# Performance work log

Hardware: AMD Instinct MI355X
Metric: run time of the kernel (lower is better)

The kernel has to match this reference:

```python
import jax, jax.numpy as jnp
import numpy as np
import math

D_MSA = 384
N_HEAD = 12
D_HID = 32


def setup_inputs() -> dict:
    key = jax.random.key(0)
    k1, k2, k3, k4, k5 = jax.random.split(key, 5)
    b, n, l = 2, 256, 384
    msa = jax.random.normal(k1, (b, n, l, D_MSA), dtype=jnp.float32)
    # xavier_uniform for (out, in) = (n_head*d_hidden, d_msa)
    fan_out, fan_in = N_HEAD * D_HID, D_MSA
    bound = math.sqrt(6.0 / (fan_in + fan_out))
    Wq = jax.random.uniform(k2, (fan_out, fan_in), jnp.float32, -bound, bound)
    Wk = jax.random.uniform(k3, (fan_out, fan_in), jnp.float32, -bound, bound)
    bq = jnp.zeros((fan_out,), jnp.float32)
    bk = jnp.zeros((fan_out,), jnp.float32)
    return {"msa": msa, "Wq": Wq, "bq": bq, "Wk": Wk, "bk": bk}


def reference(msa, Wq, bq, Wk, bk):
    b, n, l, _ = msa.shape
    scale = 1.0 / math.sqrt(D_HID)
    tar_seq = msa[:, 0]  # (b, l, d_msa) -- query comes from first MSA row
    q = (tar_seq @ Wq.T + bq).reshape(b, l, N_HEAD, D_HID) * scale  # (b,l,h,d)
    k = (msa @ Wk.T + bk).reshape(b, n, l, N_HEAD, D_HID)           # (b,n,l,h,d)
    # einsum('bqihd,bkihd->bkihq') with q==1 -> (b,n,l,h,1)
    attn = jnp.einsum('blhd,bnlhd->bnlh', q, k)[..., None]
    # softmax over MSA-depth axis (dim=1); dropout is identity at eval
    return jax.nn.softmax(attn, axis=1)
```

## Files before the change

kernel.cpp:

```cpp
#include <hip/hip_runtime.h>
#include <hip/hip_bf16.h>

#define D_MSA 384
#define NHEAD 12
#define DHID  32
#define BB    2
#define NN    256
#define LL    384
#define NBL   (BB * LL)
#define WFROW (NHEAD * D_MSA)

#define WF_OFF 0
#define WF_SZ  ((size_t)NBL * WFROW)
#define Q_OFF  (WF_OFF + WF_SZ)
#define Q_SZ   ((size_t)NBL * D_MSA)
#define CB_OFF (Q_OFF + Q_SZ)
#define CB_SZ  ((size_t)NBL * NHEAD)
#define LOG_OFF (CB_OFF + CB_SZ)
#define LOG_SZ ((size_t)NBL * NHEAD * NN)
#define WS_FLOATS (LOG_OFF + LOG_SZ)
#define WS_BYTES  (WS_FLOATS * 4)

__global__ __launch_bounds__(256)
void seqw_a1(const float* __restrict__ msa, const float* __restrict__ Wq,
             const float* __restrict__ bq, const float* __restrict__ bk,
             float* __restrict__ q_ws, float* __restrict__ cb_ws)
{
  __shared__ float tar[3][D_MSA];
  __shared__ float qs[3][D_MSA];
  const int t    = threadIdx.x;
  const int lane = t & 63;
  const int wv   = t >> 6;
  const int rowi = lane >> 4;
  const int seg  = lane & 15;
  const int bl0  = blockIdx.x * 3;
  const int b    = bl0 / LL, l0 = bl0 % LL;
  const float scale = 0.17677669529663687f;

  const float* base = msa + ((size_t)b * NN * LL + l0) * D_MSA;
  for (int i = t; i < 3 * D_MSA / 4; i += 256)
    ((float4*)tar)[i] = ((const float4*)base)[i];
  __syncthreads();

#pragma unroll 1
  for (int cc = 0; cc < 24; ++cc) {
    const int c = wv * 96 + cc * 4 + rowi;
    const float* wr = Wq + (size_t)c * D_MSA + seg * 4;
    float a0 = 0.f, a1 = 0.f, a2 = 0.f;
#pragma unroll
    for (int j = 0; j < 6; ++j) {
      float4 w4 = *(const float4*)(wr + 64 * j);
      float4 t0 = *(const float4*)&tar[0][64 * j + seg * 4];
      float4 t1 = *(const float4*)&tar[1][64 * j + seg * 4];
      float4 t2 = *(const float4*)&tar[2][64 * j + seg * 4];
      a0 = fmaf(w4.x, t0.x, a0); a0 = fmaf(w4.y, t0.y, a0);
      a0 = fmaf(w4.z, t0.z, a0); a0 = fmaf(w4.w, t0.w, a0);
      a1 = fmaf(w4.x, t1.x, a1); a1 = fmaf(w4.y, t1.y, a1);
      a1 = fmaf(w4.z, t1.z, a1); a1 = fmaf(w4.w, t1.w, a1);
      a2 = fmaf(w4.x, t2.x, a2); a2 = fmaf(w4.y, t2.y, a2);
      a2 = fmaf(w4.z, t2.z, a2); a2 = fmaf(w4.w, t2.w, a2);
    }
#pragma unroll
    for (int m = 8; m; m >>= 1) {
      a0 += __shfl_xor(a0, m);
      a1 += __shfl_xor(a1, m);
      a2 += __shfl_xor(a2, m);
    }
    if (seg == 0) {
      const float bqc = bq[c];
      const float q0 = scale * (a0 + bqc);
      const float q1 = scale * (a1 + bqc);
      const float q2 = scale * (a2 + bqc);
      qs[0][c] = q0; q_ws[(size_t)(bl0 + 0) * D_MSA + c] = q0;
      qs[1][c] = q1; q_ws[(size_t)(bl0 + 1) * D_MSA + c] = q1;
      qs[2][c] = q2; q_ws[(size_t)(bl0 + 2) * D_MSA + c] = q2;
    }
  }
  __syncthreads();

  if (t < 3 * NHEAD) {
    const int r = t / NHEAD, h = t % NHEAD;
    float s = 0.f;
#pragma unroll
    for (int d = 0; d < DHID; ++d)
      s = fmaf(qs[r][h * DHID + d], bk[h * DHID + d], s);
    cb_ws[(size_t)(bl0 + r) * NHEAD + h] = s;
  }
}

__global__ __launch_bounds__(256)
void seqw_a2(const float* __restrict__ Wk, const float* __restrict__ q_ws,
             float* __restrict__ wf_ws)
{
  __shared__ float qt[16][DHID];
  const int t   = threadIdx.x;
  const int h   = blockIdx.x % NHEAD;
  const int bl0 = (blockIdx.x / NHEAD) * 16;

  if (t < 128) {
    const int r = t >> 3, j = (t & 7) * 4;
    *(float4*)&qt[r][j] =
        *(const float4*)(q_ws + (size_t)(bl0 + r) * D_MSA + h * DHID + j);
  }
  __syncthreads();

#pragma unroll 1
  for (int pass = 0; pass < 2; ++pass) {
    const int c = pass * 256 + t;
    if (c < D_MSA) {
      float acc[16];
#pragma unroll
      for (int r = 0; r < 16; ++r) acc[r] = 0.f;
      const float* wkb = Wk + (size_t)(h * DHID) * D_MSA + c;
#pragma unroll 2
      for (int d = 0; d < DHID; d += 4) {
        const float w0 = wkb[(size_t)(d + 0) * D_MSA];
        const float w1 = wkb[(size_t)(d + 1) * D_MSA];
        const float w2 = wkb[(size_t)(d + 2) * D_MSA];
        const float w3 = wkb[(size_t)(d + 3) * D_MSA];
#pragma unroll
        for (int r = 0; r < 16; ++r) {
          float4 q4 = *(const float4*)&qt[r][d];
          acc[r] = fmaf(q4.x, w0, acc[r]);
          acc[r] = fmaf(q4.y, w1, acc[r]);
          acc[r] = fmaf(q4.z, w2, acc[r]);
          acc[r] = fmaf(q4.w, w3, acc[r]);
        }
      }
#pragma unroll
      for (int r = 0; r < 16; ++r)
        wf_ws[(size_t)(bl0 + r) * WFROW + h * D_MSA + c] = acc[r];
    }
  }
}

struct SmemB {
  float wf[NHEAD][D_MSA];
  float cb[NHEAD];
  float attn[NHEAD][128];
};

__global__ __launch_bounds__(256)
void seqw_b(const float* __restrict__ msa, const float* __restrict__ wf_ws,
            const float* __restrict__ cb_ws, float* __restrict__ log_ws)
{
  __shared__ SmemB sm;
  const int t    = threadIdx.x;
  const int lane = t & 63;
  const int wv   = t >> 6;
  const int rowi = lane >> 3;
  const int seg  = lane & 7;
  const int bid  = blockIdx.x;
  const int bl   = bid >> 1;
  const int nblk = bid & 1;
  const int b    = bl / LL;
  const int l    = bl - b * LL;
  const int h0   = 3 * wv;

  {
    const float4* src = (const float4*)(wf_ws + (size_t)bl * WFROW);
    for (int i = t; i < WFROW / 4; i += 256) ((float4*)sm.wf)[i] = src[i];
    if (t < NHEAD) sm.cb[t] = cb_ws[(size_t)bl * NHEAD + t];
  }
  __syncthreads();

  const size_t rstride = (size_t)LL * D_MSA;
  const float* lanebase =
      msa + ((size_t)(b * NN + nblk * 128 + rowi) * LL + l) * D_MSA + seg * 4;

#define LDB(buf, ch, j)                                                         \
  {                                                                             \
    _Pragma("unroll")                                                           \
    for (int g = 0; g < 8; ++g)                                                 \
      buf[g] = *(const float4*)(lanebase +                                      \
                 (size_t)((ch) * 64 + g * 8) * rstride + 32 * (j));             \
  }
#define CPB(buf, j)                                                             \
  {                                                                             \
    float4 w0 = *(const float4*)&sm.wf[h0 + 0][32 * (j) + 4 * seg];             \
    float4 w1 = *(const float4*)&sm.wf[h0 + 1][32 * (j) + 4 * seg];             \
    float4 w2 = *(const float4*)&sm.wf[h0 + 2][32 * (j) + 4 * seg];             \
    _Pragma("unroll")                                                           \
    for (int g = 0; g < 8; ++g) {                                               \
      acc[g][0] = fmaf(buf[g].x, w0.x, acc[g][0]);                              \
      acc[g][0] = fmaf(buf[g].y, w0.y, acc[g][0]);                              \
      acc[g][0] = fmaf(buf[g].z, w0.z, acc[g][0]);                              \
      acc[g][0] = fmaf(buf[g].w, w0.w, acc[g][0]);                              \
      acc[g][1] = fmaf(buf[g].x, w1.x, acc[g][1]);                              \
      acc[g][1] = fmaf(buf[g].y, w1.y, acc[g][1]);                              \
      acc[g][1] = fmaf(buf[g].z, w1.z, acc[g][1]);                              \
      acc[g][1] = fmaf(buf[g].w, w1.w, acc[g][1]);                              \
      acc[g][2] = fmaf(buf[g].x, w2.x, acc[g][2]);                              \
      acc[g][2] = fmaf(buf[g].y, w2.y, acc[g][2]);                              \
      acc[g][2] = fmaf(buf[g].z, w2.z, acc[g][2]);                              \
      acc[g][2] = fmaf(buf[g].w, w2.w, acc[g][2]);                              \
    }                                                                           \
  }

  float4 bufA[8], bufB[8];
  LDB(bufA, 0, 0)
#pragma unroll 1
  for (int ch = 0; ch < 2; ++ch) {
    float acc[8][3];
#pragma unroll
    for (int g = 0; g < 8; ++g) {
      acc[g][0] = 0.f; acc[g][1] = 0.f; acc[g][2] = 0.f;
    }
#pragma unroll 1
    for (int jj = 0; jj < 6; ++jj) {
      const int j0 = 2 * jj, j1 = 2 * jj + 1;
      LDB(bufB, ch, j1)
      CPB(bufA, j0)
      if (jj < 5)      LDB(bufA, ch, j0 + 2)
      else if (ch < 1) LDB(bufA, 1, 0)
      CPB(bufB, j1)
    }
#pragma unroll
    for (int g = 0; g < 8; ++g) {
#pragma unroll
      for (int hh = 0; hh < 3; ++hh) {
        float s = acc[g][hh];
        s += __shfl_xor(s, 4);
        s += __shfl_xor(s, 2);
        s += __shfl_xor(s, 1);
        if (seg == 0)
          sm.attn[h0 + hh][ch * 64 + g * 8 + rowi] = s + sm.cb[h0 + hh];
      }
    }
  }
  __syncthreads();

  for (int i = t; i < NHEAD * 128 / 4; i += 256) {
    const int h = i >> 5, nn4 = i & 31;
    ((float4*)log_ws)[(size_t)bl * (NHEAD * NN / 4) + h * (NN / 4) + nblk * 32 + nn4] =
        ((const float4*)sm.attn)[i];
  }
}

__global__ __launch_bounds__(256)
void seqw_c(const float* __restrict__ log_ws, float* __restrict__ out)
{
  __shared__ float at[NHEAD][NN];
  __shared__ float smax[NHEAD], sinv[NHEAD];
  const int t    = threadIdx.x;
  const int lane = t & 63;
  const int wv   = t >> 6;
  const int bl   = blockIdx.x;
  const int b    = bl / LL;
  const int l    = bl - b * LL;

  for (int i = t; i < NHEAD * NN / 4; i += 256)
    ((float4*)at)[i] = ((const float4*)log_ws)[(size_t)bl * (NHEAD * NN / 4) + i];
  __syncthreads();

#pragma unroll
  for (int jh = 0; jh < 3; ++jh) {
    const int h = wv * 3 + jh;
    float v0 = at[h][lane];
    float v1 = at[h][lane + 64];
    float v2 = at[h][lane + 128];
    float v3 = at[h][lane + 192];
    float mx = fmaxf(fmaxf(v0, v1), fmaxf(v2, v3));
#pragma unroll
    for (int m = 32; m; m >>= 1) mx = fmaxf(mx, __shfl_xor(mx, m));
    float s = __expf(v0 - mx) + __expf(v1 - mx) + __expf(v2 - mx) + __expf(v3 - mx);
#pragma unroll
    for (int m = 32; m; m >>= 1) s += __shfl_xor(s, m);
    if (lane == 0) { smax[h] = mx; sinv[h] = 1.0f / s; }
  }
  __syncthreads();

  {
    float o[NHEAD];
#pragma unroll
    for (int h = 0; h < NHEAD; ++h)
      o[h] = __expf(at[h][t] - smax[h]) * sinv[h];
    float* ob = out + ((size_t)(b * NN + t) * LL + l) * NHEAD;
    ((float4*)ob)[0] = make_float4(o[0], o[1], o[2],  o[3]);
    ((float4*)ob)[1] = make_float4(o[4], o[5], o[6],  o[7]);
    ((float4*)ob)[2] = make_float4(o[8], o[9], o[10], o[11]);
  }
}

struct SmemF {
  float tar[D_MSA];
  float q[D_MSA];
  float wf[NHEAD][D_MSA];
  float cb[NHEAD];
  float smax[NHEAD];
  float sinv[NHEAD];
  float attn[NHEAD][NN];
};

__global__ __launch_bounds__(512, 2)
void seqw_fused_fb(const float* __restrict__ msa, const float* __restrict__ Wq,
                   const float* __restrict__ bq, const float* __restrict__ Wk,
                   const float* __restrict__ bk, float* __restrict__ out)
{
  __shared__ SmemF sm;
  const int t    = threadIdx.x;
  const int lane = t & 63;
  const int wv   = t >> 6;
  const int rowi = lane >> 4;
  const int seg  = lane & 15;
  const int bl   = blockIdx.x;
  const int b    = bl / LL;
  const int l    = bl - b * LL;
  const float scale = 0.17677669529663687f;

  const float* targ = msa + ((size_t)(b * NN) * LL + l) * D_MSA;
  if (t < 96) ((float4*)sm.tar)[t] = ((const float4*)targ)[t];
  __syncthreads();

  {
    float2 t2[3];
#pragma unroll
    for (int p = 0; p < 3; ++p) t2[p] = *(const float2*)&sm.tar[2 * lane + 128 * p];
#pragma unroll 1
    for (int j = 0; j < 48; ++j) {
      const int r = wv * 48 + j;
      const float* wr = Wq + (size_t)r * D_MSA;
      float s = 0.f;
#pragma unroll
      for (int p = 0; p < 3; ++p) {
        float2 w2 = *(const float2*)&wr[2 * lane + 128 * p];
        s = fmaf(t2[p].x, w2.x, s);
        s = fmaf(t2[p].y, w2.y, s);
      }
#pragma unroll
      for (int m = 32; m; m >>= 1) s += __shfl_xor(s, m);
      if (lane == 0) sm.q[r] = scale * (s + bq[r]);
    }
  }
  __syncthreads();

  if (t < D_MSA) {
    const int c = t;
    float a[NHEAD];
#pragma unroll
    for (int h = 0; h < NHEAD; ++h) a[h] = 0.f;
#pragma unroll 1
    for (int d = 0; d < DHID; ++d) {
#pragma unroll
      for (int h = 0; h < NHEAD; ++h)
        a[h] = fmaf(sm.q[h * DHID + d], Wk[(size_t)(h * DHID + d) * D_MSA + c], a[h]);
    }
#pragma unroll
    for (int h = 0; h < NHEAD; ++h) sm.wf[h][c] = a[h];
  }
  if (t < NHEAD) {
    float s = 0.f;
#pragma unroll
    for (int d = 0; d < DHID; ++d) s = fmaf(sm.q[t * DHID + d], bk[t * DHID + d], s);
    sm.cb[t] = s;
  }
  __syncthreads();

  const size_t rstride = (size_t)LL * D_MSA;
  const float* lanebase =
      msa + ((size_t)(b * NN + wv * 32 + rowi) * LL + l) * D_MSA + seg * 4;

#define LDF(buf, base, j)                                                       \
  {                                                                             \
    buf[0] = *(const float4*)((base) + 64 * (j));                               \
    buf[1] = *(const float4*)((base) + 4 * rstride + 64 * (j));                 \
  }
#define CPF(buf, j)                                                             \
  {                                                                             \
    _Pragma("unroll")                                                           \
    for (int h = 0; h < NHEAD; ++h) {                                           \
      float4 w4 = *(const float4*)&sm.wf[h][64 * (j) + 4 * seg];                \
      acc[0][h] = fmaf(buf[0].x, w4.x, acc[0][h]);                              \
      acc[0][h] = fmaf(buf[0].y, w4.y, acc[0][h]);                              \
      acc[0][h] = fmaf(buf[0].z, w4.z, acc[0][h]);                              \
      acc[0][h] = fmaf(buf[0].w, w4.w, acc[0][h]);                              \
      acc[1][h] = fmaf(buf[1].x, w4.x, acc[1][h]);                              \
      acc[1][h] = fmaf(buf[1].y, w4.y, acc[1][h]);                              \
      acc[1][h] = fmaf(buf[1].z, w4.z, acc[1][h]);                              \
      acc[1][h] = fmaf(buf[1].w, w4.w, acc[1][h]);                              \
    }                                                                           \
  }

  const float* pcur = lanebase;
  float4 bufA[2], bufB[2];
  LDF(bufA, pcur, 0)
#pragma unroll 1
  for (int ch = 0; ch < 4; ++ch) {
    float acc[2][NHEAD];
#pragma unroll
    for (int g = 0; g < 2; ++g)
#pragma unroll
      for (int h = 0; h < NHEAD; ++h) acc[g][h] = 0.f;
    const float* pnext = pcur + 8 * rstride;
    LDF(bufB, pcur, 1)  CPF(bufA, 0)
    LDF(bufA, pcur, 2)  CPF(bufB, 1)
    LDF(bufB, pcur, 3)  CPF(bufA, 2)
    LDF(bufA, pcur, 4)  CPF(bufB, 3)
    LDF(bufB, pcur, 5)  CPF(bufA, 4)
    if (ch < 3) LDF(bufA, pnext, 0)
    CPF(bufB, 5)
#pragma unroll
    for (int g = 0; g < 2; ++g) {
      const int n = wv * 32 + ch * 8 + g * 4 + rowi;
#pragma unroll
      for (int h = 0; h < NHEAD; ++h) {
        float s = acc[g][h];
        s += __shfl_xor(s, 8);
        s += __shfl_xor(s, 4);
        s += __shfl_xor(s, 2);
        s += __shfl_xor(s, 1);
        if (seg == 0) sm.attn[h][n] = s + sm.cb[h];
      }
    }
    pcur = pnext;
  }
  __syncthreads();

  if (wv < 6) {
#pragma unroll
    for (int jh = 0; jh < 2; ++jh) {
      const int h = wv * 2 + jh;
      float v0 = sm.attn[h][lane];
      float v1 = sm.attn[h][lane + 64];
      float v2 = sm.attn[h][lane + 128];
      float v3 = sm.attn[h][lane + 192];
      float mx = fmaxf(fmaxf(v0, v1), fmaxf(v2, v3));
#pragma unroll
      for (int m = 32; m; m >>= 1) mx = fmaxf(mx, __shfl_xor(mx, m));
      float s = __expf(v0 - mx) + __expf(v1 - mx) + __expf(v2 - mx) + __expf(v3 - mx);
#pragma unroll
      for (int m = 32; m; m >>= 1) s += __shfl_xor(s, m);
      if (lane == 0) { sm.smax[h] = mx; sm.sinv[h] = 1.0f / s; }
    }
  }
  __syncthreads();

  if (t < NN) {
    float o[NHEAD];
#pragma unroll
    for (int h = 0; h < NHEAD; ++h)
      o[h] = __expf(sm.attn[h][t] - sm.smax[h]) * sm.sinv[h];
    float* ob = out + ((size_t)(b * NN + t) * LL + l) * NHEAD;
    ((float4*)ob)[0] = make_float4(o[0], o[1], o[2],  o[3]);
    ((float4*)ob)[1] = make_float4(o[4], o[5], o[6],  o[7]);
    ((float4*)ob)[2] = make_float4(o[8], o[9], o[10], o[11]);
  }
}

extern "C" void kernel_launch(void* const* d_in, const int* in_sizes, int n_in,
                              void* d_out, int out_size, void* d_ws, size_t ws_size,
                              hipStream_t stream) {
  const float* msa = (const float*)d_in[0];
  const float* Wq  = (const float*)d_in[1];
  const float* bq  = (const float*)d_in[2];
  const float* Wk  = (const float*)d_in[3];
  const float* bk  = (const float*)d_in[4];
  float* out = (float*)d_out;

  if (ws_size >= WS_BYTES) {
    float* ws     = (float*)d_ws;
    float* wf_ws  = ws + WF_OFF;
    float* q_ws   = ws + Q_OFF;
    float* cb_ws  = ws + CB_OFF;
    float* log_ws = ws + LOG_OFF;
    seqw_a1<<<dim3(NBL / 3), dim3(256), 0, stream>>>(msa, Wq, bq, bk, q_ws, cb_ws);
    seqw_a2<<<dim3(NHEAD * (NBL / 16)), dim3(256), 0, stream>>>(Wk, q_ws, wf_ws);
    seqw_b<<<dim3(NBL * 2), dim3(256), 0, stream>>>(msa, wf_ws, cb_ws, log_ws);
    seqw_c<<<dim3(NBL), dim3(256), 0, stream>>>(log_ws, out);
  } else {
    seqw_fused_fb<<<dim3(NBL), dim3(512), 0, stream>>>(msa, Wq, bq, Wk, bk, out);
  }
}
```

Measured before the change: 153.9 us.

## Fuse query projection and Wk-folding kernels, remap block order in later kernels

Merges the two pre-pass kernels into one: each block now computes 4 query rows and then folds them through Wk for all 12 heads directly from shared memory. This removes the q workspace round-trip and one kernel launch. The cost is fewer blocks (192) and Wk reuse across only 4 rows instead of 16, which means more Wk reads overall. Separately, seqw_b and seqw_c permute block indices with an interleave by 8, apparently so that consecutive blocks land on different XCDs or L2 slices.

```diff
diff --git a/kernel.cpp b/kernel.cpp
--- a/kernel.cpp
+++ b/kernel.cpp
@@ -12,9 +12,7 @@
 
 #define WF_OFF 0
 #define WF_SZ  ((size_t)NBL * WFROW)
-#define Q_OFF  (WF_OFF + WF_SZ)
-#define Q_SZ   ((size_t)NBL * D_MSA)
-#define CB_OFF (Q_OFF + Q_SZ)
+#define CB_OFF (WF_OFF + WF_SZ)
 #define CB_SZ  ((size_t)NBL * NHEAD)
 #define LOG_OFF (CB_OFF + CB_SZ)
 #define LOG_SZ ((size_t)NBL * NHEAD * NN)
@@ -22,23 +20,24 @@
 #define WS_BYTES  (WS_FLOATS * 4)
 
 __global__ __launch_bounds__(256)
-void seqw_a1(const float* __restrict__ msa, const float* __restrict__ Wq,
-             const float* __restrict__ bq, const float* __restrict__ bk,
-             float* __restrict__ q_ws, float* __restrict__ cb_ws)
+void seqw_a(const float* __restrict__ msa, const float* __restrict__ Wq,
+            const float* __restrict__ bq, const float* __restrict__ Wk,
+            const float* __restrict__ bk,
+            float* __restrict__ wf_ws, float* __restrict__ cb_ws)
 {
-  __shared__ float tar[3][D_MSA];
-  __shared__ float qs[3][D_MSA];
+  __shared__ float tar[4][D_MSA];
+  __shared__ float qs[4][D_MSA];
   const int t    = threadIdx.x;
   const int lane = t & 63;
   const int wv   = t >> 6;
   const int rowi = lane >> 4;
   const int seg  = lane & 15;
-  const int bl0  = blockIdx.x * 3;
+  const int bl0  = blockIdx.x * 4;
   const int b    = bl0 / LL, l0 = bl0 % LL;
   const float scale = 0.17677669529663687f;
 
   const float* base = msa + ((size_t)b * NN * LL + l0) * D_MSA;
-  for (int i = t; i < 3 * D_MSA / 4; i += 256)
+  for (int i = t; i < 4 * D_MSA / 4; i += 256)
     ((float4*)tar)[i] = ((const float4*)base)[i];
   __syncthreads();
 
@@ -46,39 +45,33 @@
   for (int cc = 0; cc < 24; ++cc) {
     const int c = wv * 96 + cc * 4 + rowi;
     const float* wr = Wq + (size_t)c * D_MSA + seg * 4;
-    float a0 = 0.f, a1 = 0.f, a2 = 0.f;
+    float a[4];
+#pragma unroll
+    for (int r = 0; r < 4; ++r) a[r] = 0.f;
 #pragma unroll
     for (int j = 0; j < 6; ++j) {
       float4 w4 = *(const float4*)(wr + 64 * j);
-      float4 t0 = *(const float4*)&tar[0][64 * j + seg * 4];
-      float4 t1 = *(const float4*)&tar[1][64 * j + seg * 4];
-      float4 t2 = *(const float4*)&tar[2][64 * j + seg * 4];
-      a0 = fmaf(w4.x, t0.x, a0); a0 = fmaf(w4.y, t0.y, a0);
-      a0 = fmaf(w4.z, t0.z, a0); a0 = fmaf(w4.w, t0.w, a0);
-      a1 = fmaf(w4.x, t1.x, a1); a1 = fmaf(w4.y, t1.y, a1);
-      a1 = fmaf(w4.z, t1.z, a1); a1 = fmaf(w4.w, t1.w, a1);
-      a2 = fmaf(w4.x, t2.x, a2); a2 = fmaf(w4.y, t2.y, a2);
-      a2 = fmaf(w4.z, t2.z, a2); a2 = fmaf(w4.w, t2.w, a2);
+#pragma unroll
+      for (int r = 0; r < 4; ++r) {
+        float4 tv = *(const float4*)&tar[r][64 * j + seg * 4];
+        a[r] = fmaf(w4.x, tv.x, a[r]); a[r] = fmaf(w4.y, tv.y, a[r]);
+        a[r] = fmaf(w4.z, tv.z, a[r]); a[r] = fmaf(w4.w, tv.w, a[r]);
+      }
     }
 #pragma unroll
     for (int m = 8; m; m >>= 1) {
-      a0 += __shfl_xor(a0, m);
-      a1 += __shfl_xor(a1, m);
-      a2 += __shfl_xor(a2, m);
+#pragma unroll
+      for (int r = 0; r < 4; ++r) a[r] += __shfl_xor(a[r], m);
     }
     if (seg == 0) {
       const float bqc = bq[c];
-      const float q0 = scale * (a0 + bqc);
-      const float q1 = scale * (a1 + bqc);
-      const float q2 = scale * (a2 + bqc);
-      qs[0][c] = q0; q_ws[(size_t)(bl0 + 0) * D_MSA + c] = q0;
-      qs[1][c] = q1; q_ws[(size_t)(bl0 + 1) * D_MSA + c] = q1;
-      qs[2][c] = q2; q_ws[(size_t)(bl0 + 2) * D_MSA + c] = q2;
-    }
-  }
-  __syncthreads();
-
-  if (t < 3 * NHEAD) {
+#pragma unroll
+      for (int r = 0; r < 4; ++r) qs[r][c] = scale * (a[r] + bqc);
+    }
+  }
+  __syncthreads();
+
+  if (t < 4 * NHEAD) {
     const int r = t / NHEAD, h = t % NHEAD;
     float s = 0.f;
 #pragma unroll
@@ -86,50 +79,28 @@
       s = fmaf(qs[r][h * DHID + d], bk[h * DHID + d], s);
     cb_ws[(size_t)(bl0 + r) * NHEAD + h] = s;
   }
-}
-
-__global__ __launch_bounds__(256)
-void seqw_a2(const float* __restrict__ Wk, const float* __restrict__ q_ws,
-             float* __restrict__ wf_ws)
-{
-  __shared__ float qt[16][DHID];
-  const int t   = threadIdx.x;
-  const int h   = blockIdx.x % NHEAD;
-  const int bl0 = (blockIdx.x / NHEAD) * 16;
-
-  if (t < 128) {
-    const int r = t >> 3, j = (t & 7) * 4;
-    *(float4*)&qt[r][j] =
-        *(const float4*)(q_ws + (size_t)(bl0 + r) * D_MSA + h * DHID + j);
-  }
-  __syncthreads();
 
 #pragma unroll 1
   for (int pass = 0; pass < 2; ++pass) {
     const int c = pass * 256 + t;
     if (c < D_MSA) {
-      float acc[16];
-#pragma unroll
-      for (int r = 0; r < 16; ++r) acc[r] = 0.f;
-      const float* wkb = Wk + (size_t)(h * DHID) * D_MSA + c;
-#pragma unroll 2
-      for (int d = 0; d < DHID; d += 4) {
-        const float w0 = wkb[(size_t)(d + 0) * D_MSA];
-        const float w1 = wkb[(size_t)(d + 1) * D_MSA];
-        const float w2 = wkb[(size_t)(d + 2) * D_MSA];
-        const float w3 = wkb[(size_t)(d + 3) * D_MSA];
-#pragma unroll
-        for (int r = 0; r < 16; ++r) {
-          float4 q4 = *(const float4*)&qt[r][d];
-          acc[r] = fmaf(q4.x, w0, acc[r]);
-          acc[r] = fmaf(q4.y, w1, acc[r]);
-          acc[r] = fmaf(q4.z, w2, acc[r]);
-          acc[r] = fmaf(q4.w, w3, acc[r]);
+#pragma unroll 1
+      for (int h = 0; h < NHEAD; ++h) {
+        float acc4[4];
+#pragma unroll
+        for (int r = 0; r < 4; ++r) acc4[r] = 0.f;
+        const float* wkb = Wk + (size_t)(h * DHID) * D_MSA + c;
+#pragma unroll 4
+        for (int d = 0; d < DHID; ++d) {
+          const float w = wkb[(size_t)d * D_MSA];
+#pragma unroll
+          for (int r = 0; r < 4; ++r)
+            acc4[r] = fmaf(qs[r][h * DHID + d], w, acc4[r]);
         }
+#pragma unroll
+        for (int r = 0; r < 4; ++r)
+          wf_ws[(size_t)(bl0 + r) * WFROW + h * D_MSA + c] = acc4[r];
       }
-#pragma unroll
-      for (int r = 0; r < 16; ++r)
-        wf_ws[(size_t)(bl0 + r) * WFROW + h * D_MSA + c] = acc[r];
     }
   }
 }
@@ -150,7 +121,8 @@
   const int wv   = t >> 6;
   const int rowi = lane >> 3;
   const int seg  = lane & 7;
-  const int bid  = blockIdx.x;
+  const int i0   = blockIdx.x;
+  const int bid  = (i0 & 7) * (NBL * 2 / 8) + (i0 >> 3);
   const int bl   = bid >> 1;
   const int nblk = bid & 1;
   const int b    = bl / LL;
@@ -245,7 +217,8 @@
   const int t    = threadIdx.x;
   const int lane = t & 63;
   const int wv   = t >> 6;
-  const int bl   = blockIdx.x;
+  const int i0   = blockIdx.x;
+  const int bl   = (i0 & 7) * (NBL / 8) + (i0 >> 3);
   const int b    = bl / LL;
   const int l    = bl - b * LL;
 
@@ -460,11 +433,9 @@
   if (ws_size >= WS_BYTES) {
     float* ws     = (float*)d_ws;
     float* wf_ws  = ws + WF_OFF;
-    float* q_ws   = ws + Q_OFF;
     float* cb_ws  = ws + CB_OFF;
     float* log_ws = ws + LOG_OFF;
-    seqw_a1<<<dim3(NBL / 3), dim3(256), 0, stream>>>(msa, Wq, bq, bk, q_ws, cb_ws);
-    seqw_a2<<<dim3(NHEAD * (NBL / 16)), dim3(256), 0, stream>>>(Wk, q_ws, wf_ws);
+    seqw_a<<<dim3(NBL / 4), dim3(256), 0, stream>>>(msa, Wq, bq, Wk, bk, wf_ws, cb_ws);
     seqw_b<<<dim3(NBL * 2), dim3(256), 0, stream>>>(msa, wf_ws, cb_ws, log_ws);
     seqw_c<<<dim3(NBL), dim3(256), 0, stream>>>(log_ws, out);
   } else {
```

After: 188.7 us. 22.6% more time.

## Fuse softmax kernel into logits kernel, one block per (b,l) covering all rows

Applied to the files above, without the earlier changes.

The logits kernel now handles all 256 MSA rows for each (b,l) in one block, instead of splitting them across two blocks. It then computes the softmax over depth directly from shared memory and writes the output. This removes the separate softmax kernel launch and the global round-trip of the logits workspace. The cost is half as many blocks (768) with double the serial work per block, which reduces parallelism and the ability to hide latency on the main msa-streaming kernel.

```diff
diff --git a/kernel.cpp b/kernel.cpp
--- a/kernel.cpp
+++ b/kernel.cpp
@@ -16,9 +16,7 @@
 #define Q_SZ   ((size_t)NBL * D_MSA)
 #define CB_OFF (Q_OFF + Q_SZ)
 #define CB_SZ  ((size_t)NBL * NHEAD)
-#define LOG_OFF (CB_OFF + CB_SZ)
-#define LOG_SZ ((size_t)NBL * NHEAD * NN)
-#define WS_FLOATS (LOG_OFF + LOG_SZ)
+#define WS_FLOATS (CB_OFF + CB_SZ)
 #define WS_BYTES  (WS_FLOATS * 4)
 
 __global__ __launch_bounds__(256)
@@ -137,12 +135,14 @@
 struct SmemB {
   float wf[NHEAD][D_MSA];
   float cb[NHEAD];
-  float attn[NHEAD][128];
+  float attn[NHEAD][NN];
+  float smax[NHEAD];
+  float sinv[NHEAD];
 };
 
 __global__ __launch_bounds__(256)
 void seqw_b(const float* __restrict__ msa, const float* __restrict__ wf_ws,
-            const float* __restrict__ cb_ws, float* __restrict__ log_ws)
+            const float* __restrict__ cb_ws, float* __restrict__ out)
 {
   __shared__ SmemB sm;
   const int t    = threadIdx.x;
@@ -150,9 +150,7 @@
   const int wv   = t >> 6;
   const int rowi = lane >> 3;
   const int seg  = lane & 7;
-  const int bid  = blockIdx.x;
-  const int bl   = bid >> 1;
-  const int nblk = bid & 1;
+  const int bl   = blockIdx.x;
   const int b    = bl / LL;
   const int l    = bl - b * LL;
   const int h0   = 3 * wv;
@@ -166,7 +164,7 @@
 
   const size_t rstride = (size_t)LL * D_MSA;
   const float* lanebase =
-      msa + ((size_t)(b * NN + nblk * 128 + rowi) * LL + l) * D_MSA + seg * 4;
+      msa + ((size_t)(b * NN + rowi) * LL + l) * D_MSA + seg * 4;
 
 #define LDB(buf, ch, j)                                                         \
   {                                                                             \
@@ -200,7 +198,7 @@
   float4 bufA[8], bufB[8];
   LDB(bufA, 0, 0)
 #pragma unroll 1
-  for (int ch = 0; ch < 2; ++ch) {
+  for (int ch = 0; ch < 4; ++ch) {
     float acc[8][3];
 #pragma unroll
     for (int g = 0; g < 8; ++g) {
@@ -212,7 +210,7 @@
       LDB(bufB, ch, j1)
       CPB(bufA, j0)
       if (jj < 5)      LDB(bufA, ch, j0 + 2)
-      else if (ch < 1) LDB(bufA, 1, 0)
+      else if (ch < 3) LDB(bufA, ch + 1, 0)
       CPB(bufB, j1)
     }
 #pragma unroll
@@ -230,43 +228,20 @@
   }
   __syncthreads();
 
-  for (int i = t; i < NHEAD * 128 / 4; i += 256) {
-    const int h = i >> 5, nn4 = i & 31;
-    ((float4*)log_ws)[(size_t)bl * (NHEAD * NN / 4) + h * (NN / 4) + nblk * 32 + nn4] =
-        ((const float4*)sm.attn)[i];
-  }
-}
-
-__global__ __launch_bounds__(256)
-void seqw_c(const float* __restrict__ log_ws, float* __restrict__ out)
-{
-  __shared__ float at[NHEAD][NN];
-  __shared__ float smax[NHEAD], sinv[NHEAD];
-  const int t    = threadIdx.x;
-  const int lane = t & 63;
-  const int wv   = t >> 6;
-  const int bl   = blockIdx.x;
-  const int b    = bl / LL;
-  const int l    = bl - b * LL;
-
-  for (int i = t; i < NHEAD * NN / 4; i += 256)
-    ((float4*)at)[i] = ((const float4*)log_ws)[(size_t)bl * (NHEAD * NN / 4) + i];
-  __syncthreads();
-
 #pragma unroll
   for (int jh = 0; jh < 3; ++jh) {
     const int h = wv * 3 + jh;
-    float v0 = at[h][lane];
-    float v1 = at[h][lane + 64];
-    float v2 = at[h][lane + 128];
-    float v3 = at[h][lane + 192];
+    float v0 = sm.attn[h][lane];
+    float v1 = sm.attn[h][lane + 64];
+    float v2 = sm.attn[h][lane + 128];
+    float v3 = sm.attn[h][lane + 192];
     float mx = fmaxf(fmaxf(v0, v1), fmaxf(v2, v3));
 #pragma unroll
     for (int m = 32; m; m >>= 1) mx = fmaxf(mx, __shfl_xor(mx, m));
     float s = __expf(v0 - mx) + __expf(v1 - mx) + __expf(v2 - mx) + __expf(v3 - mx);
 #pragma unroll
     for (int m = 32; m; m >>= 1) s += __shfl_xor(s, m);
-    if (lane == 0) { smax[h] = mx; sinv[h] = 1.0f / s; }
+    if (lane == 0) { sm.smax[h] = mx; sm.sinv[h] = 1.0f / s; }
   }
   __syncthreads();
 
@@ -274,7 +249,7 @@
     float o[NHEAD];
 #pragma unroll
     for (int h = 0; h < NHEAD; ++h)
-      o[h] = __expf(at[h][t] - smax[h]) * sinv[h];
+      o[h] = __expf(sm.attn[h][t] - sm.smax[h]) * sm.sinv[h];
     float* ob = out + ((size_t)(b * NN + t) * LL + l) * NHEAD;
     ((float4*)ob)[0] = make_float4(o[0], o[1], o[2],  o[3]);
     ((float4*)ob)[1] = make_float4(o[4], o[5], o[6],  o[7]);
@@ -458,15 +433,13 @@
   float* out = (float*)d_out;
 
   if (ws_size >= WS_BYTES) {
-    float* ws     = (float*)d_ws;
-    float* wf_ws  = ws + WF_OFF;
-    float* q_ws   = ws + Q_OFF;
-    float* cb_ws  = ws + CB_OFF;
-    float* log_ws = ws + LOG_OFF;
+    float* ws    = (float*)d_ws;
+    float* wf_ws = ws + WF_OFF;
+    float* q_ws  = ws + Q_OFF;
+    float* cb_ws = ws + CB_OFF;
     seqw_a1<<<dim3(NBL / 3), dim3(256), 0, stream>>>(msa, Wq, bq, bk, q_ws, cb_ws);
     seqw_a2<<<dim3(NHEAD * (NBL / 16)), dim3(256), 0, stream>>>(Wk, q_ws, wf_ws);
-    seqw_b<<<dim3(NBL * 2), dim3(256), 0, stream>>>(msa, wf_ws, cb_ws, log_ws);
-    seqw_c<<<dim3(NBL), dim3(256), 0, stream>>>(log_ws, out);
+    seqw_b<<<dim3(NBL), dim3(256), 0, stream>>>(msa, wf_ws, cb_ws, out);
   } else {
     seqw_fused_fb<<<dim3(NBL), dim3(512), 0, stream>>>(msa, Wq, bq, Wk, bk, out);
   }
```

Result: slower. 160.4 us (+4.3%).

## Split seqw_b work into quarter-row blocks with 6 heads per wave

Applied to the files above, without the earlier changes.

Reorganizes the main msa-streaming kernel so each block handles 64 MSA rows instead of 128, doubling the grid. Each wave now covers 32 rows and 6 heads instead of 64 rows and 3 heads, which halves the in-flight load buffers per thread and cuts the two-chunk loop. The intent is more parallelism and more blocks to hide memory latency. In exchange, the per-block staging of the 18 KB wf row into shared memory is repeated twice as often.

```diff
diff --git a/kernel.cpp b/kernel.cpp
--- a/kernel.cpp
+++ b/kernel.cpp
@@ -134,106 +134,94 @@
   }
 }
 
-struct SmemB {
-  float wf[NHEAD][D_MSA];
-  float cb[NHEAD];
-  float attn[NHEAD][128];
-};
-
 __global__ __launch_bounds__(256)
 void seqw_b(const float* __restrict__ msa, const float* __restrict__ wf_ws,
             const float* __restrict__ cb_ws, float* __restrict__ log_ws)
 {
-  __shared__ SmemB sm;
+  __shared__ float wf_s[NHEAD][D_MSA];
+  __shared__ float cb_s[NHEAD];
+  __shared__ float attn_s[NHEAD][64];
   const int t    = threadIdx.x;
   const int lane = t & 63;
   const int wv   = t >> 6;
+  const int hg   = wv & 1;
+  const int rq   = wv >> 1;
+  const int h0   = 6 * hg;
   const int rowi = lane >> 3;
   const int seg  = lane & 7;
   const int bid  = blockIdx.x;
-  const int bl   = bid >> 1;
-  const int nblk = bid & 1;
+  const int bl   = bid >> 2;
+  const int nq   = bid & 3;
   const int b    = bl / LL;
   const int l    = bl - b * LL;
-  const int h0   = 3 * wv;
 
   {
     const float4* src = (const float4*)(wf_ws + (size_t)bl * WFROW);
-    for (int i = t; i < WFROW / 4; i += 256) ((float4*)sm.wf)[i] = src[i];
-    if (t < NHEAD) sm.cb[t] = cb_ws[(size_t)bl * NHEAD + t];
+    for (int i = t; i < WFROW / 4; i += 256) ((float4*)wf_s)[i] = src[i];
+    if (t < NHEAD) cb_s[t] = cb_ws[(size_t)bl * NHEAD + t];
   }
   __syncthreads();
 
   const size_t rstride = (size_t)LL * D_MSA;
   const float* lanebase =
-      msa + ((size_t)(b * NN + nblk * 128 + rowi) * LL + l) * D_MSA + seg * 4;
-
-#define LDB(buf, ch, j)                                                         \
+      msa + ((size_t)(b * NN + nq * 64 + rq * 32 + rowi) * LL + l) * D_MSA + seg * 4;
+
+#define LDB(buf, j)                                                             \
   {                                                                             \
     _Pragma("unroll")                                                           \
-    for (int g = 0; g < 8; ++g)                                                 \
-      buf[g] = *(const float4*)(lanebase +                                      \
-                 (size_t)((ch) * 64 + g * 8) * rstride + 32 * (j));             \
+    for (int g = 0; g < 4; ++g)                                                 \
+      buf[g] = *(const float4*)(lanebase + (size_t)(g * 8) * rstride + 32 * (j)); \
   }
 #define CPB(buf, j)                                                             \
   {                                                                             \
-    float4 w0 = *(const float4*)&sm.wf[h0 + 0][32 * (j) + 4 * seg];             \
-    float4 w1 = *(const float4*)&sm.wf[h0 + 1][32 * (j) + 4 * seg];             \
-    float4 w2 = *(const float4*)&sm.wf[h0 + 2][32 * (j) + 4 * seg];             \
     _Pragma("unroll")                                                           \
-    for (int g = 0; g < 8; ++g) {                                               \
-      acc[g][0] = fmaf(buf[g].x, w0.x, acc[g][0]);                              \
-      acc[g][0] = fmaf(buf[g].y, w0.y, acc[g][0]);                              \
-      acc[g][0] = fmaf(buf[g].z, w0.z, acc[g][0]);                              \
-      acc[g][0] = fmaf(buf[g].w, w0.w, acc[g][0]);                              \
-      acc[g][1] = fmaf(buf[g].x, w1.x, acc[g][1]);                              \
-      acc[g][1] = fmaf(buf[g].y, w1.y, acc[g][1]);                              \
-      acc[g][1] = fmaf(buf[g].z, w1.z, acc[g][1]);                              \
-      acc[g][1] = fmaf(buf[g].w, w1.w, acc[g][1]);                              \
-      acc[g][2] = fmaf(buf[g].x, w2.x, acc[g][2]);                              \
-      acc[g][2] = fmaf(buf[g].y, w2.y, acc[g][2]);                              \
-      acc[g][2] = fmaf(buf[g].z, w2.z, acc[g][2]);                              \
-      acc[g][2] = fmaf(buf[g].w, w2.w, acc[g][2]);                              \
+    for (int hh = 0; hh < 6; ++hh) {                                            \
+      float4 w4 = *(const float4*)&wf_s[h0 + hh][32 * (j) + 4 * seg];           \
+      _Pragma("unroll")                                                         \
+      for (int g = 0; g < 4; ++g) {                                             \
+        acc[g][hh] = fmaf(buf[g].x, w4.x, acc[g][hh]);                          \
+        acc[g][hh] = fmaf(buf[g].y, w4.y, acc[g][hh]);                          \
+        acc[g][hh] = fmaf(buf[g].z, w4.z, acc[g][hh]);                          \
+        acc[g][hh] = fmaf(buf[g].w, w4.w, acc[g][hh]);                          \
+      }                                                                         \
     }                                                                           \
   }
 
-  float4 bufA[8], bufB[8];
-  LDB(bufA, 0, 0)
-#pragma unroll 1
-  for (int ch = 0; ch < 2; ++ch) {
-    float acc[8][3];
-#pragma unroll
-    for (int g = 0; g < 8; ++g) {
-      acc[g][0] = 0.f; acc[g][1] = 0.f; acc[g][2] = 0.f;
-    }
-#pragma unroll 1
-    for (int jj = 0; jj < 6; ++jj) {
-      const int j0 = 2 * jj, j1 = 2 * jj + 1;
-      LDB(bufB, ch, j1)
-      CPB(bufA, j0)
-      if (jj < 5)      LDB(bufA, ch, j0 + 2)
-      else if (ch < 1) LDB(bufA, 1, 0)
-      CPB(bufB, j1)
-    }
-#pragma unroll
-    for (int g = 0; g < 8; ++g) {
-#pragma unroll
-      for (int hh = 0; hh < 3; ++hh) {
-        float s = acc[g][hh];
-        s += __shfl_xor(s, 4);
-        s += __shfl_xor(s, 2);
-        s += __shfl_xor(s, 1);
-        if (seg == 0)
-          sm.attn[h0 + hh][ch * 64 + g * 8 + rowi] = s + sm.cb[h0 + hh];
-      }
-    }
-  }
-  __syncthreads();
-
-  for (int i = t; i < NHEAD * 128 / 4; i += 256) {
-    const int h = i >> 5, nn4 = i & 31;
-    ((float4*)log_ws)[(size_t)bl * (NHEAD * NN / 4) + h * (NN / 4) + nblk * 32 + nn4] =
-        ((const float4*)sm.attn)[i];
+  float acc[4][6];
+#pragma unroll
+  for (int g = 0; g < 4; ++g)
+#pragma unroll
+    for (int hh = 0; hh < 6; ++hh) acc[g][hh] = 0.f;
+
+  float4 bufA[4], bufB[4];
+  LDB(bufA, 0)
+#pragma unroll 1
+  for (int jj = 0; jj < 6; ++jj) {
+    const int j0 = 2 * jj, j1 = 2 * jj + 1;
+    LDB(bufB, j1)
+    CPB(bufA, j0)
+    if (jj < 5) LDB(bufA, j0 + 2)
+    CPB(bufB, j1)
+  }
+
+#pragma unroll
+  for (int g = 0; g < 4; ++g) {
+#pragma unroll
+    for (int hh = 0; hh < 6; ++hh) {
+      float s = acc[g][hh];
+      s += __shfl_xor(s, 4);
+      s += __shfl_xor(s, 2);
+      s += __shfl_xor(s, 1);
+      if (seg == 0)
+        attn_s[h0 + hh][rq * 32 + g * 8 + rowi] = s + cb_s[h0 + hh];
+    }
+  }
+  __syncthreads();
+
+  for (int i = t; i < NHEAD * 64 / 4; i += 256) {
+    const int h = i >> 4, r4 = i & 15;
+    ((float4*)log_ws)[(size_t)bl * (NHEAD * NN / 4) + h * (NN / 4) + nq * 16 + r4] =
+        ((const float4*)attn_s)[i];
   }
 }
 
@@ -465,7 +453,7 @@
     float* log_ws = ws + LOG_OFF;
     seqw_a1<<<dim3(NBL / 3), dim3(256), 0, stream>>>(msa, Wq, bq, bk, q_ws, cb_ws);
     seqw_a2<<<dim3(NHEAD * (NBL / 16)), dim3(256), 0, stream>>>(Wk, q_ws, wf_ws);
-    seqw_b<<<dim3(NBL * 2), dim3(256), 0, stream>>>(msa, wf_ws, cb_ws, log_ws);
+    seqw_b<<<dim3(NBL * 4), dim3(256), 0, stream>>>(msa, wf_ws, cb_ws, log_ws);
     seqw_c<<<dim3(NBL), dim3(256), 0, stream>>>(log_ws, out);
   } else {
     seqw_fused_fb<<<dim3(NBL), dim3(512), 0, stream>>>(msa, Wq, bq, Wk, bk, out);
```

New measurement: 129.7 us. 15.7% less time.
